# Optimization experiments

Hardware: AMD Instinct MI355X
Metric: run time of the kernel (lower is better)

Reference implementation:

```python
import jax, jax.numpy as jnp
import numpy as np

N_NODES = 50000
N_EDGES = 800000
N_GRAPHS = 128
IN_DIM = 128
HID = 128
OUT = 64
N_CONV = 4
BN_EPS = 1e-5


def setup_inputs() -> dict:
    key = jax.random.key(0)
    ks = jax.random.split(key, 12)
    h = jax.random.normal(ks[0], (N_NODES, IN_DIM), jnp.float32)
    edge_src = jax.random.randint(ks[1], (N_EDGES,), 0, N_NODES)
    edge_dst = jax.random.randint(ks[2], (N_EDGES,), 0, N_NODES)
    graph_ids = jnp.sort(jax.random.randint(ks[3], (N_NODES,), 0, N_GRAPHS))
    s1 = 1.0 / np.sqrt(IN_DIM)
    W1 = jax.random.uniform(ks[4], (N_CONV, IN_DIM, HID), jnp.float32, -s1, s1)
    W2 = jax.random.uniform(ks[5], (N_CONV, HID, HID), jnp.float32, -s1, s1)
    bn1_g = jnp.ones((N_CONV, HID), jnp.float32)
    bn1_b = jnp.zeros((N_CONV, HID), jnp.float32)
    bn2_g = jnp.ones((N_CONV, HID), jnp.float32)
    bn2_b = jnp.zeros((N_CONV, HID), jnp.float32)
    predW = jax.random.uniform(ks[6], (5, HID, OUT), jnp.float32, -s1, s1)
    predb = jnp.zeros((5, OUT), jnp.float32)
    return dict(h=h, edge_src=edge_src, edge_dst=edge_dst, graph_ids=graph_ids,
                W1=W1, bn1_g=bn1_g, bn1_b=bn1_b, W2=W2, bn2_g=bn2_g, bn2_b=bn2_b,
                predW=predW, predb=predb)


def _batchnorm(x, g, b):
    # training-mode batchnorm over the node dimension (biased variance, as torch)
    m = jnp.mean(x, axis=0)
    v = jnp.mean(jnp.square(x - m), axis=0)
    return (x - m) * jax.lax.rsqrt(v + BN_EPS) * g + b


def reference(h, edge_src, edge_dst, graph_ids, W1, bn1_g, bn1_b, W2, bn2_g, bn2_b, predW, predb):
    hidden_rep = [h]
    for i in range(N_CONV):
        # GINConv, eps=0: aggregate neighbor sum, add self, apply MLP
        agg = jax.ops.segment_sum(h[edge_src], edge_dst, num_segments=N_NODES)
        z = agg + h  # [N, d]
        z = jnp.matmul(z, W1[i])
        z = jax.nn.relu(_batchnorm(z, bn1_g[i], bn1_b[i]))
        z = jnp.matmul(z, W2[i])
        # outer batchnorm + relu
        h = jax.nn.relu(_batchnorm(z, bn2_g[i], bn2_b[i]))
        hidden_rep.append(h)
    score = jnp.zeros((N_GRAPHS, OUT), jnp.float32)
    for i, hi in enumerate(hidden_rep):
        pooled = jax.ops.segment_sum(hi, graph_ids, num_segments=N_GRAPHS)  # [G, d]
        score = score + jnp.matmul(pooled, predW[i]) + predb[i]
    return score
```

## Files before the change

kernel.cpp:

```cpp
#include <hip/hip_runtime.h>

#define NN 50000
#define NE 800000
#define NG 128
#define DIM 128
#define OUTD 64
#define NCONV 4
#define NB 196
#define BN_EPS 1e-5f

typedef __attribute__((ext_vector_type(8))) short short8;
typedef __attribute__((ext_vector_type(4))) float f32x4;
union BF8 { uint4 u; short8 s; };

__device__ inline unsigned f2bf(float f) {
    unsigned u = __float_as_uint(f);
    return (u + 0x7FFFu + ((u >> 16) & 1u)) >> 16;
}
__device__ inline float bf_lo(unsigned u) { return __uint_as_float(u << 16); }
__device__ inline float bf_hi(unsigned u) { return __uint_as_float(u & 0xFFFF0000u); }

__global__ __launch_bounds__(256) void k_degree(const int* __restrict__ dst,
                                                int* __restrict__ deg)
{
    int e = blockIdx.x * 256 + threadIdx.x;
    if (e < NE) atomicAdd(&deg[dst[e]], 1);
}

__global__ __launch_bounds__(256) void k_scan1(const int* __restrict__ deg,
                                               int* __restrict__ bsum)
{
    __shared__ int part[256];
    int t = threadIdx.x, idx = blockIdx.x * 256 + t;
    int v = (idx < NN) ? deg[idx] : 0;
    part[t] = v;
    __syncthreads();
    #pragma unroll
    for (int off = 1; off < 256; off <<= 1) {
        int u = (t >= off) ? part[t - off] : 0;
        __syncthreads();
        part[t] += u;
        __syncthreads();
    }
    if (t == 255) bsum[blockIdx.x] = part[255];
}

__global__ __launch_bounds__(256) void k_scan2(const int* __restrict__ bsum,
                                               int* __restrict__ boff)
{
    __shared__ int part[256];
    int t = threadIdx.x;
    int v = (t < NB) ? bsum[t] : 0;
    part[t] = v;
    __syncthreads();
    #pragma unroll
    for (int off = 1; off < 256; off <<= 1) {
        int u = (t >= off) ? part[t - off] : 0;
        __syncthreads();
        part[t] += u;
        __syncthreads();
    }
    if (t < NB) boff[t] = part[t] - v;
}

__global__ __launch_bounds__(256) void k_scan3(const int* __restrict__ deg,
                                               const int* __restrict__ boff,
                                               int* __restrict__ rowptr,
                                               int* __restrict__ cursor)
{
    __shared__ int part[256];
    int t = threadIdx.x, idx = blockIdx.x * 256 + t;
    int v = (idx < NN) ? deg[idx] : 0;
    part[t] = v;
    __syncthreads();
    #pragma unroll
    for (int off = 1; off < 256; off <<= 1) {
        int u = (t >= off) ? part[t - off] : 0;
        __syncthreads();
        part[t] += u;
        __syncthreads();
    }
    if (idx < NN) {
        int excl = part[t] - v + boff[blockIdx.x];
        rowptr[idx] = excl;
        cursor[idx] = excl;
    }
    if (idx == 0) rowptr[NN] = NE;
}

__global__ __launch_bounds__(256) void k_fill(const int* __restrict__ src,
                                              const int* __restrict__ dst,
                                              int* __restrict__ cursor,
                                              int* __restrict__ csr)
{
    int e = blockIdx.x * 256 + threadIdx.x;
    if (e >= NE) return;
    int pos = atomicAdd(&cursor[dst[e]], 1);
    csr[pos] = src[e];
}

__global__ __launch_bounds__(256) void k_bounds(const int* __restrict__ gid,
                                                int* __restrict__ gstart)
{
    int n = blockIdx.x * 256 + threadIdx.x;
    if (n >= NN) return;
    int g = gid[n];
    int gp = (n == 0) ? -1 : gid[n - 1];
    for (int x = gp + 1; x <= g; ++x) gstart[x] = n;
    if (n == NN - 1)
        for (int x = g + 1; x <= NG; ++x) gstart[x] = NN;
}

__global__ __launch_bounds__(256) void k_wprep(const float* __restrict__ W1,
                                               const float* __restrict__ W2,
                                               unsigned short* __restrict__ Wbf)
{
    int tid = blockIdx.x * 256 + threadIdx.x;
    int l   = tid & 63;
    int ctg = (tid >> 6) & 7;
    int kk  = (tid >> 9) & 3;
    int mat = tid >> 11;
    const float* Ws = (mat < 4) ? (W1 + (size_t)mat * DIM * DIM)
                                : (W2 + (size_t)(mat - 4) * DIM * DIM);
    int col = ctg * 16 + (l & 15);
    int k0  = kk * 32 + (l >> 4) * 8;
    unsigned sh[8];
    #pragma unroll
    for (int j = 0; j < 8; ++j) sh[j] = f2bf(Ws[(size_t)(k0 + j) * DIM + col]);
    uint4 pk;
    pk.x = sh[0] | (sh[1] << 16); pk.y = sh[2] | (sh[3] << 16);
    pk.z = sh[4] | (sh[5] << 16); pk.w = sh[6] | (sh[7] << 16);
    ((uint4*)Wbf)[tid] = pk;
}

__global__ __launch_bounds__(256) void k_cvt(const float* __restrict__ in,
                                             unsigned short* __restrict__ outb)
{
    int idx = blockIdx.x * 256 + threadIdx.x;
    if (idx >= NN * DIM / 4) return;
    float4 v = ((const float4*)in)[idx];
    uint2 pk;
    pk.x = f2bf(v.x) | (f2bf(v.y) << 16);
    pk.y = f2bf(v.z) | (f2bf(v.w) << 16);
    ((uint2*)outb)[idx] = pk;
}

__device__ inline void bn_affine4(const float* __restrict__ sumP,
                                  const float* __restrict__ sqP,
                                  const float* __restrict__ gP,
                                  const float* __restrict__ bP,
                                  int ch0, float4& av, float4& cv)
{
    const float invM = 1.f / (float)NN;
    #pragma unroll
    for (int j = 0; j < 4; ++j) {
        int ch = ch0 + j;
        float m = sumP[ch] * invM;
        float var = sqP[ch] * invM - m * m;
        float s = gP[ch] * rsqrtf(var + BN_EPS);
        (&av.x)[j] = s;
        (&cv.x)[j] = bP[ch] - m * s;
    }
}

__device__ inline float4 aff_relu(float4 v, const float4 av, const float4 cv)
{
    v.x = fmaxf(fmaf(v.x, av.x, cv.x), 0.f);
    v.y = fmaxf(fmaf(v.y, av.y, cv.y), 0.f);
    v.z = fmaxf(fmaf(v.z, av.z, cv.z), 0.f);
    v.w = fmaxf(fmaf(v.w, av.w, cv.w), 0.f);
    return v;
}

template<bool AFFINE, bool WRITEH, bool INBF16>
__global__ __launch_bounds__(256) void k_poolseg(
    const void* __restrict__ z_,
    const float* __restrict__ sumP, const float* __restrict__ sqP,
    const float* __restrict__ gP, const float* __restrict__ bP,
    const int* __restrict__ gstart, float* __restrict__ pooled,
    unsigned short* __restrict__ hbf)
{
    const int g = blockIdx.x >> 2, split = blockIdx.x & 3;
    const int s = gstart[g], e = gstart[g + 1];
    const int len = e - s;
    const int chunk = (len + 3) >> 2;
    const int rs = s + split * chunk;
    const int re = min(e, rs + chunk);
    const int c4 = threadIdx.x & 31, rl = threadIdx.x >> 5;
    float4 av, cv;
    if (AFFINE) bn_affine4(sumP, sqP, gP, bP, c4 * 4, av, cv);
    float4 acc = make_float4(0.f, 0.f, 0.f, 0.f);
    for (int r = rs + rl; r < re; r += 8) {
        float4 v;
        if (INBF16) {
            uint2 w = ((const uint2*)z_)[(size_t)r * 32 + c4];
            v = make_float4(bf_lo(w.x), bf_hi(w.x), bf_lo(w.y), bf_hi(w.y));
        } else {
            v = ((const float4*)z_)[(size_t)r * 32 + c4];
        }
        if (AFFINE) v = aff_relu(v, av, cv);
        if (WRITEH) {
            uint2 pk;
            pk.x = f2bf(v.x) | (f2bf(v.y) << 16);
            pk.y = f2bf(v.z) | (f2bf(v.w) << 16);
            ((uint2*)(hbf + (size_t)r * DIM))[c4] = pk;
        }
        acc.x += v.x; acc.y += v.y; acc.z += v.z; acc.w += v.w;
    }
    __shared__ float4 red[8][32];
    red[rl][c4] = acc;
    __syncthreads();
    if (rl == 0) {
        float4 s4 = red[0][c4];
        #pragma unroll
        for (int r8 = 1; r8 < 8; ++r8) {
            float4 u = red[r8][c4];
            s4.x += u.x; s4.y += u.y; s4.z += u.z; s4.w += u.w;
        }
        float* p = pooled + (size_t)g * DIM + c4 * 4;
        atomicAdd(p + 0, s4.x);
        atomicAdd(p + 1, s4.y);
        atomicAdd(p + 2, s4.z);
        atomicAdd(p + 3, s4.w);
    }
}

template<bool GATHER, bool AFFINE>
__global__ __launch_bounds__(256) void k_gemm_mfma(
    const unsigned short* __restrict__ Xb,
    const int* __restrict__ rowptr, const int* __restrict__ csr,
    const float* __restrict__ sumP, const float* __restrict__ sqP,
    const float* __restrict__ gP, const float* __restrict__ bP,
    const unsigned short* __restrict__ Wbf,
    unsigned short* __restrict__ Z,
    float* __restrict__ colsum, float* __restrict__ colsq)
{
    __shared__ unsigned short a_lds[16 * 520];
    const int t = threadIdx.x;
    const int row0 = blockIdx.x * 64;
    const int q = t & 15;

    float av[8], cv[8];
    if (AFFINE) {
        const float invM = 1.f / (float)NN;
        #pragma unroll
        for (int j = 0; j < 8; ++j) {
            int ch = q * 8 + j;
            float m = sumP[ch] * invM;
            float var = sqP[ch] * invM - m * m;
            float sc = gP[ch] * rsqrtf(var + BN_EPS);
            av[j] = sc; cv[j] = bP[ch] - m * sc;
        }
    }

    const uint4* hp4 = (const uint4*)Xb;
    #pragma unroll
    for (int it = 0; it < 4; ++it) {
        int row = (t >> 4) + it * 16;
        int grow = row0 + row;
        uint4 pk = make_uint4(0, 0, 0, 0);
        if (grow < NN) {
            float a[8];
            uint4 v = hp4[(size_t)grow * 16 + q];
            a[0] = bf_lo(v.x); a[1] = bf_hi(v.x);
            a[2] = bf_lo(v.y); a[3] = bf_hi(v.y);
            a[4] = bf_lo(v.z); a[5] = bf_hi(v.z);
            a[6] = bf_lo(v.w); a[7] = bf_hi(v.w);
            if (GATHER) {
                int p = rowptr[grow], end = rowptr[grow + 1];
                for (; p + 2 <= end; p += 2) {
                    int s0 = csr[p], s1 = csr[p + 1];
                    uint4 u0 = hp4[(size_t)s0 * 16 + q];
                    uint4 u1 = hp4[(size_t)s1 * 16 + q];
                    a[0] += bf_lo(u0.x) + bf_lo(u1.x);
                    a[1] += bf_hi(u0.x) + bf_hi(u1.x);
                    a[2] += bf_lo(u0.y) + bf_lo(u1.y);
                    a[3] += bf_hi(u0.y) + bf_hi(u1.y);
                    a[4] += bf_lo(u0.z) + bf_lo(u1.z);
                    a[5] += bf_hi(u0.z) + bf_hi(u1.z);
                    a[6] += bf_lo(u0.w) + bf_lo(u1.w);
                    a[7] += bf_hi(u0.w) + bf_hi(u1.w);
                }
                if (p < end) {
                    uint4 u = hp4[(size_t)csr[p] * 16 + q];
                    a[0] += bf_lo(u.x); a[1] += bf_hi(u.x);
                    a[2] += bf_lo(u.y); a[3] += bf_hi(u.y);
                    a[4] += bf_lo(u.z); a[5] += bf_hi(u.z);
                    a[6] += bf_lo(u.w); a[7] += bf_hi(u.w);
                }
            }
            if (AFFINE) {
                #pragma unroll
                for (int j = 0; j < 8; ++j)
                    a[j] = fmaxf(fmaf(a[j], av[j], cv[j]), 0.f);
            }
            pk.x = f2bf(a[0]) | (f2bf(a[1]) << 16);
            pk.y = f2bf(a[2]) | (f2bf(a[3]) << 16);
            pk.z = f2bf(a[4]) | (f2bf(a[5]) << 16);
            pk.w = f2bf(a[6]) | (f2bf(a[7]) << 16);
        }
        int g = (row >> 4) * 4 + (q >> 2);
        int l = (row & 15) + (q & 3) * 16;
        *(uint4*)(a_lds + g * 520 + l * 8) = pk;
    }
    __syncthreads();

    const int w = t >> 6, lane = t & 63;
    const int rh = w >> 1, ch = w & 1;
    f32x4 acc[2][4];
    #pragma unroll
    for (int i = 0; i < 2; ++i)
        #pragma unroll
        for (int j = 0; j < 4; ++j) acc[i][j] = 0;

    const uint4* Wb = (const uint4*)Wbf;
    #pragma unroll
    for (int kk = 0; kk < 4; ++kk) {
        BF8 a[2], b[4];
        #pragma unroll
        for (int rti = 0; rti < 2; ++rti) {
            int g = (rh * 2 + rti) * 4 + kk;
            a[rti].u = *(const uint4*)(a_lds + g * 520 + lane * 8);
        }
        #pragma unroll
        for (int ct = 0; ct < 4; ++ct)
            b[ct].u = Wb[(kk * 8 + ch * 4 + ct) * 64 + lane];
        #pragma unroll
        for (int rti = 0; rti < 2; ++rti)
            #pragma unroll
            for (int ct = 0; ct < 4; ++ct)
                acc[rti][ct] = __builtin_amdgcn_mfma_f32_16x16x32_bf16(
                    a[rti].s, b[ct].s, acc[rti][ct], 0, 0, 0);
    }

    float ps[4] = {0.f, 0.f, 0.f, 0.f}, pq[4] = {0.f, 0.f, 0.f, 0.f};
    #pragma unroll
    for (int rti = 0; rti < 2; ++rti) {
        #pragma unroll
        for (int r = 0; r < 4; ++r) {
            int grow = row0 + rh * 32 + rti * 16 + (lane >> 4) * 4 + r;
            if (grow < NN) {
                #pragma unroll
                for (int ct = 0; ct < 4; ++ct) {
                    float v = acc[rti][ct][r];
                    Z[(size_t)grow * DIM + ch * 64 + ct * 16 + (lane & 15)] =
                        (unsigned short)f2bf(v);
                    ps[ct] += v;
                    pq[ct] += v * v;
                }
            }
        }
    }
    __syncthreads();
    float* red = (float*)a_lds;
    red[t] = 0.f;
    __syncthreads();
    #pragma unroll
    for (int ct = 0; ct < 4; ++ct) {
        int col = ch * 64 + ct * 16 + (lane & 15);
        atomicAdd(&red[col], ps[ct]);
        atomicAdd(&red[128 + col], pq[ct]);
    }
    __syncthreads();
    if (t < DIM) {
        atomicAdd(colsum + t, red[t]);
        atomicAdd(colsq + t, red[128 + t]);
    }
}

__global__ __launch_bounds__(320) void k_score(const float* __restrict__ pooled,
                                               const float* __restrict__ predW,
                                               const float* __restrict__ predb,
                                               float* __restrict__ out)
{
    __shared__ float red[5][OUTD];
    const int g = blockIdx.x;
    const int w = threadIdx.x >> 6;
    const int o = threadIdx.x & 63;
    const float* pr = pooled + (size_t)w * NG * DIM + (size_t)g * DIM;
    const float* Wp = predW + (size_t)w * DIM * OUTD;
    float acc = predb[w * OUTD + o];
    #pragma unroll 8
    for (int k = 0; k < DIM; ++k) acc = fmaf(pr[k], Wp[k * OUTD + o], acc);
    red[w][o] = acc;
    __syncthreads();
    if (threadIdx.x < OUTD) {
        float s = red[0][o] + red[1][o] + red[2][o] + red[3][o] + red[4][o];
        out[(size_t)g * OUTD + o] = s;
    }
}

extern "C" void kernel_launch(void* const* d_in, const int* in_sizes, int n_in,
                              void* d_out, int out_size, void* d_ws, size_t ws_size,
                              hipStream_t stream)
{
    const float* h     = (const float*)d_in[0];
    const int*   esrc  = (const int*)d_in[1];
    const int*   edst  = (const int*)d_in[2];
    const int*   gid   = (const int*)d_in[3];
    const float* W1    = (const float*)d_in[4];
    const float* bn1g  = (const float*)d_in[5];
    const float* bn1b  = (const float*)d_in[6];
    const float* W2    = (const float*)d_in[7];
    const float* bn2g  = (const float*)d_in[8];
    const float* bn2b  = (const float*)d_in[9];
    const float* predW = (const float*)d_in[10];
    const float* predb = (const float*)d_in[11];
    float* out = (float*)d_out;

    float* ws = (float*)d_ws;
    const size_t NF = (size_t)NN * DIM;
    float* pooled = ws;
    float* stats  = pooled + 5 * NG * DIM;

    unsigned short* hbf  = (unsigned short*)(stats + NCONV * 1024);
    unsigned short* z1b  = hbf + NF;
    unsigned short* z2b  = z1b + NF;
    unsigned short* Wbf  = z2b + NF;
    int* ideg   = (int*)(Wbf + 8 * 16384);
    int* rowptr = ideg + NN;
    int* cursor = rowptr + NN + 1;
    int* csr    = cursor + NN;
    int* gstart = csr + NE;
    int* bsum   = gstart + NG + 1;
    int* boff   = bsum + NB;

    hipMemsetAsync(pooled, 0, (5 * NG * DIM + NCONV * 1024) * sizeof(float), stream);
    hipMemsetAsync(ideg, 0, NN * sizeof(int), stream);

    k_wprep<<<64, 256, 0, stream>>>(W1, W2, Wbf);
    k_cvt<<<(NN * DIM / 4 + 255) / 256, 256, 0, stream>>>(h, hbf);
    k_degree<<<(NE + 255) / 256, 256, 0, stream>>>(edst, ideg);
    k_scan1<<<NB, 256, 0, stream>>>(ideg, bsum);
    k_scan2<<<1, 256, 0, stream>>>(bsum, boff);
    k_scan3<<<NB, 256, 0, stream>>>(ideg, boff, rowptr, cursor);
    k_fill<<<(NE + 255) / 256, 256, 0, stream>>>(esrc, edst, cursor, csr);
    k_bounds<<<(NN + 255) / 256, 256, 0, stream>>>(gid, gstart);

    k_poolseg<false, false, false><<<NG * 4, 256, 0, stream>>>(
        h, nullptr, nullptr, nullptr, nullptr, gstart, pooled, nullptr);

    const int GB = (NN + 63) / 64;
    for (int i = 0; i < NCONV; ++i) {
        float* st = stats + i * 1024;
        k_gemm_mfma<true, false><<<GB, 256, 0, stream>>>(
            hbf, rowptr, csr, nullptr, nullptr, nullptr, nullptr,
            Wbf + (size_t)i * 16384, z1b, st, st + 128);
        k_gemm_mfma<false, true><<<GB, 256, 0, stream>>>(
            z1b, nullptr, nullptr, st, st + 128, bn1g + i * DIM, bn1b + i * DIM,
            Wbf + (size_t)(4 + i) * 16384, z2b, st + 512, st + 640);
        if (i < NCONV - 1)
            k_poolseg<true, true, true><<<NG * 4, 256, 0, stream>>>(
                z2b, st + 512, st + 640, bn2g + i * DIM, bn2b + i * DIM,
                gstart, pooled + (size_t)(i + 1) * NG * DIM, hbf);
        else
            k_poolseg<true, false, true><<<NG * 4, 256, 0, stream>>>(
                z2b, st + 512, st + 640, bn2g + i * DIM, bn2b + i * DIM,
                gstart, pooled + (size_t)(i + 1) * NG * DIM, nullptr);
    }

    k_score<<<NG, 320, 0, stream>>>(pooled, predW, predb, out);
}
```

Before: 618.4 us.

## Gather neighbors with four edge lanes per row and shuffle-reduce

The neighbor aggregation inside the GEMM kernel now gives each wave 16 rows in turn. Each row's edge list is split across four 16-lane groups, and the partial sums are combined with cross-lane shuffles. Before, one 16-lane group walked a row's whole edge list alone. This gives more independent gathers in flight per row, which targets the latency of the irregular loads, at the cost of shuffle work and idle lanes when rows have few edges. The non-gather, non-affine path also skips the bf16 unpack and repack and copies the raw data.

```diff
diff --git a/kernel.cpp b/kernel.cpp
--- a/kernel.cpp
+++ b/kernel.cpp
@@ -238,70 +238,102 @@
     __shared__ unsigned short a_lds[16 * 520];
     const int t = threadIdx.x;
     const int row0 = blockIdx.x * 64;
-    const int q = t & 15;
-
-    float av[8], cv[8];
-    if (AFFINE) {
-        const float invM = 1.f / (float)NN;
-        #pragma unroll
-        for (int j = 0; j < 8; ++j) {
-            int ch = q * 8 + j;
-            float m = sumP[ch] * invM;
-            float var = sqP[ch] * invM - m * m;
-            float sc = gP[ch] * rsqrtf(var + BN_EPS);
-            av[j] = sc; cv[j] = bP[ch] - m * sc;
-        }
-    }
-
     const uint4* hp4 = (const uint4*)Xb;
-    #pragma unroll
-    for (int it = 0; it < 4; ++it) {
-        int row = (t >> 4) + it * 16;
-        int grow = row0 + row;
-        uint4 pk = make_uint4(0, 0, 0, 0);
-        if (grow < NN) {
-            float a[8];
-            uint4 v = hp4[(size_t)grow * 16 + q];
-            a[0] = bf_lo(v.x); a[1] = bf_hi(v.x);
-            a[2] = bf_lo(v.y); a[3] = bf_hi(v.y);
-            a[4] = bf_lo(v.z); a[5] = bf_hi(v.z);
-            a[6] = bf_lo(v.w); a[7] = bf_hi(v.w);
-            if (GATHER) {
+
+    if (GATHER) {
+        const int wv = t >> 6, lane = t & 63;
+        const int j = lane >> 4, q = lane & 15;
+        for (int rr = 0; rr < 16; ++rr) {
+            int row = wv * 16 + rr;
+            int grow = row0 + row;
+            bool valid = grow < NN;
+            float a[8] = {0.f, 0.f, 0.f, 0.f, 0.f, 0.f, 0.f, 0.f};
+            if (valid) {
+                if (j == 0) {
+                    uint4 v = hp4[(size_t)grow * 16 + q];
+                    a[0] = bf_lo(v.x); a[1] = bf_hi(v.x);
+                    a[2] = bf_lo(v.y); a[3] = bf_hi(v.y);
+                    a[4] = bf_lo(v.z); a[5] = bf_hi(v.z);
+                    a[6] = bf_lo(v.w); a[7] = bf_hi(v.w);
+                }
                 int p = rowptr[grow], end = rowptr[grow + 1];
-                for (; p + 2 <= end; p += 2) {
-                    int s0 = csr[p], s1 = csr[p + 1];
-                    uint4 u0 = hp4[(size_t)s0 * 16 + q];
-                    uint4 u1 = hp4[(size_t)s1 * 16 + q];
-                    a[0] += bf_lo(u0.x) + bf_lo(u1.x);
-                    a[1] += bf_hi(u0.x) + bf_hi(u1.x);
-                    a[2] += bf_lo(u0.y) + bf_lo(u1.y);
-                    a[3] += bf_hi(u0.y) + bf_hi(u1.y);
-                    a[4] += bf_lo(u0.z) + bf_lo(u1.z);
-                    a[5] += bf_hi(u0.z) + bf_hi(u1.z);
-                    a[6] += bf_lo(u0.w) + bf_lo(u1.w);
-                    a[7] += bf_hi(u0.w) + bf_hi(u1.w);
-                }
-                if (p < end) {
-                    uint4 u = hp4[(size_t)csr[p] * 16 + q];
+                for (; p + 4 <= end; p += 4) {
+                    int s = csr[p + j];
+                    uint4 u = hp4[(size_t)s * 16 + q];
                     a[0] += bf_lo(u.x); a[1] += bf_hi(u.x);
                     a[2] += bf_lo(u.y); a[3] += bf_hi(u.y);
                     a[4] += bf_lo(u.z); a[5] += bf_hi(u.z);
                     a[6] += bf_lo(u.w); a[7] += bf_hi(u.w);
                 }
-            }
-            if (AFFINE) {
-                #pragma unroll
-                for (int j = 0; j < 8; ++j)
-                    a[j] = fmaxf(fmaf(a[j], av[j], cv[j]), 0.f);
-            }
-            pk.x = f2bf(a[0]) | (f2bf(a[1]) << 16);
-            pk.y = f2bf(a[2]) | (f2bf(a[3]) << 16);
-            pk.z = f2bf(a[4]) | (f2bf(a[5]) << 16);
-            pk.w = f2bf(a[6]) | (f2bf(a[7]) << 16);
-        }
-        int g = (row >> 4) * 4 + (q >> 2);
-        int l = (row & 15) + (q & 3) * 16;
-        *(uint4*)(a_lds + g * 520 + l * 8) = pk;
+                if (p + j < end) {
+                    int s = csr[p + j];
+                    uint4 u = hp4[(size_t)s * 16 + q];
+                    a[0] += bf_lo(u.x); a[1] += bf_hi(u.x);
+                    a[2] += bf_lo(u.y); a[3] += bf_hi(u.y);
+                    a[4] += bf_lo(u.z); a[5] += bf_hi(u.z);
+                    a[6] += bf_lo(u.w); a[7] += bf_hi(u.w);
+                }
+            }
+            #pragma unroll
+            for (int i = 0; i < 8; ++i) {
+                a[i] += __shfl_xor(a[i], 16);
+                a[i] += __shfl_xor(a[i], 32);
+            }
+            if (j == 0) {
+                uint4 pk = make_uint4(0, 0, 0, 0);
+                if (valid) {
+                    pk.x = f2bf(a[0]) | (f2bf(a[1]) << 16);
+                    pk.y = f2bf(a[2]) | (f2bf(a[3]) << 16);
+                    pk.z = f2bf(a[4]) | (f2bf(a[5]) << 16);
+                    pk.w = f2bf(a[6]) | (f2bf(a[7]) << 16);
+                }
+                int g = (row >> 4) * 4 + (q >> 2);
+                int l = (row & 15) + (q & 3) * 16;
+                *(uint4*)(a_lds + g * 520 + l * 8) = pk;
+            }
+        }
+    } else {
+        const int q = t & 15;
+        float av[8], cv[8];
+        if (AFFINE) {
+            const float invM = 1.f / (float)NN;
+            #pragma unroll
+            for (int jj = 0; jj < 8; ++jj) {
+                int ch = q * 8 + jj;
+                float m = sumP[ch] * invM;
+                float var = sqP[ch] * invM - m * m;
+                float sc = gP[ch] * rsqrtf(var + BN_EPS);
+                av[jj] = sc; cv[jj] = bP[ch] - m * sc;
+            }
+        }
+        #pragma unroll
+        for (int it = 0; it < 4; ++it) {
+            int row = (t >> 4) + it * 16;
+            int grow = row0 + row;
+            uint4 pk = make_uint4(0, 0, 0, 0);
+            if (grow < NN) {
+                uint4 v = hp4[(size_t)grow * 16 + q];
+                if (AFFINE) {
+                    float a[8];
+                    a[0] = bf_lo(v.x); a[1] = bf_hi(v.x);
+                    a[2] = bf_lo(v.y); a[3] = bf_hi(v.y);
+                    a[4] = bf_lo(v.z); a[5] = bf_hi(v.z);
+                    a[6] = bf_lo(v.w); a[7] = bf_hi(v.w);
+                    #pragma unroll
+                    for (int jj = 0; jj < 8; ++jj)
+                        a[jj] = fmaxf(fmaf(a[jj], av[jj], cv[jj]), 0.f);
+                    pk.x = f2bf(a[0]) | (f2bf(a[1]) << 16);
+                    pk.y = f2bf(a[2]) | (f2bf(a[3]) << 16);
+                    pk.z = f2bf(a[4]) | (f2bf(a[5]) << 16);
+                    pk.w = f2bf(a[6]) | (f2bf(a[7]) << 16);
+                } else {
+                    pk = v;
+                }
+            }
+            int g = (row >> 4) * 4 + (q >> 2);
+            int l = (row & 15) + (q & 3) * 16;
+            *(uint4*)(a_lds + g * 520 + l * 8) = pk;
+        }
     }
     __syncthreads();
 
```

New measurement: 713.5 us. +15.4%, slower.
